# Kernel tuning notes

Measured on AMD Instinct MI355X. Metric: run time of the kernel, lower is better.

The kernel has to match this reference:

```python
import jax, jax.numpy as jnp
import numpy as np

B, DIM, H, W = 8, 128, 64, 64
HEADS = 8
NUMS = DIM // HEADS   # 16
OUT = 256

def setup_inputs() -> dict:
    key = jax.random.key(0)
    k1, k2, k3, k4, k5 = jax.random.split(key, 5)
    x = jax.random.normal(k1, (B, DIM, H, W), dtype=jnp.float32)
    # per-group 1x1 conv (num_heads -> 1): weight [nums, heads], bias [nums]
    W1 = jax.random.normal(k2, (NUMS, HEADS), dtype=jnp.float32) * (1.0 / np.sqrt(HEADS))
    b1 = jax.random.normal(k3, (NUMS,), dtype=jnp.float32) * 0.01
    # final 1x1 conv (nums*dim -> out_dim): weight [out, nums*dim], bias [out]
    W2 = jax.random.normal(k4, (OUT, NUMS * DIM), dtype=jnp.float32) * (1.0 / np.sqrt(NUMS * DIM))
    b2 = jax.random.normal(k5, (OUT,), dtype=jnp.float32) * 0.01
    return {"x": x, "W1": W1, "b1": b1, "W2": W2, "b2": b2}

def reference(x, W1, b1, W2, b2):
    B_, C, H_, W_ = x.shape
    # split channels into nums groups of num_heads: [B, nums, heads, H, W]
    xg = x.reshape(B_, NUMS, HEADS, H_, W_)
    # per-group 1x1 conv to 1 channel + ReLU -> attention maps [B, nums, H, W]
    fm = jax.nn.relu(jnp.einsum('bghxy,gh->bgxy', xg, W1) + b1[None, :, None, None])
    # broadcast-multiply each map against full x, concat -> [B, nums*dim, H, W]
    feat = (fm[:, :, None, :, :] * x[:, None, :, :, :]).reshape(B_, NUMS * C, H_, W_)
    # final 1x1 conv -> [B, out_dim, H, W]
    out = jnp.einsum('bcxy,oc->boxy', feat, W2) + b2[None, :, None, None]
    return out
```

## Files before the change

kernel.cpp:

```cpp
#include <hip/hip_runtime.h>

typedef float f32x4 __attribute__((ext_vector_type(4)));
typedef int   i32x4 __attribute__((ext_vector_type(4)));
typedef unsigned int u32;

#define HW_N  4096
#define C_N   128
#define G_N   16
#define K_N   2048
#define O_N   256
#define BN    128

__device__ __forceinline__ u32 pack4(float a, float b, float c, float d, float inv) {
  int q0 = (int)rintf(a * inv), q1 = (int)rintf(b * inv);
  int q2 = (int)rintf(c * inv), q3 = (int)rintf(d * inv);
  return (u32)(q0 & 255) | ((u32)(q1 & 255) << 8) |
         ((u32)(q2 & 255) << 16) | ((u32)(q3 & 255) << 24);
}

__global__ void w2q_k(const float* __restrict__ W2, char* __restrict__ w2q,
                      float* __restrict__ sw) {
  int o = (blockIdx.x * 256 + threadIdx.x) >> 6;
  int l = threadIdx.x & 63;
  const f32x4* rp = reinterpret_cast<const f32x4*>(W2 + (size_t)o * K_N + l * 32);
  float v[32]; float am = 0.f;
#pragma unroll
  for (int q = 0; q < 8; ++q) {
    f32x4 t = rp[q];
#pragma unroll
    for (int j = 0; j < 4; ++j) { v[q * 4 + j] = t[j]; am = fmaxf(am, fabsf(t[j])); }
  }
#pragma unroll
  for (int s = 1; s < 64; s <<= 1) am = fmaxf(am, __shfl_xor(am, s, 64));
  am = fmaxf(am, 1e-30f);
  float inv = 127.0f / am;
  if (l == 0) sw[o] = am / 127.0f;
#pragma unroll
  for (int c = 0; c < 2; ++c) {
    int k0 = l * 32 + c * 16;
    u32 pk[4];
#pragma unroll
    for (int q = 0; q < 4; ++q)
      pk[q] = pack4(v[c * 16 + q * 4 + 0], v[c * 16 + q * 4 + 1],
                    v[c * 16 + q * 4 + 2], v[c * 16 + q * 4 + 3], inv);
    int frag = (o >> 4) * 32 + (k0 >> 7) * 2 + ((k0 >> 6) & 1);
    int lif  = (o & 15) + ((k0 >> 4) & 3) * 16;
    *reinterpret_cast<i32x4*>(w2q + (size_t)frag * 1024 + lif * 16) =
        *reinterpret_cast<i32x4*>(pk);
  }
}

__launch_bounds__(256, 2)
__global__ void ccattn_main_k(const float* __restrict__ x,
                              const float* __restrict__ W1,
                              const float* __restrict__ b1,
                              const char* __restrict__ w2q,
                              const float* __restrict__ sw,
                              const float* __restrict__ b2,
                              float* __restrict__ out) {
  __shared__ char  qxT[BN * 128];
  __shared__ float fmT[G_N][BN];
  __shared__ float sxT[BN];
  __shared__ float lmax[2][BN];

  const int tid = threadIdx.x;
  const int bid = blockIdx.x;
  const int mt  = bid >> 8;
  const int pt  = bid & 255;
  const int b   = pt >> 5;
  const int px0 = (pt & 31) * BN;

  const float* xb = x + (size_t)b * C_N * HW_N + px0;

  const int px    = tid & 127;
  const int chalf = tid >> 7;
  float v[8][8];
  {
    float am = 0.f;
#pragma unroll
    for (int gg = 0; gg < 8; ++gg) {
      const int g  = chalf * 8 + gg;
      const int c0 = g * 8;
      float s = b1[g];
#pragma unroll
      for (int j = 0; j < 8; ++j) {
        float t = xb[(size_t)(c0 + j) * HW_N + px];
        v[gg][j] = t;
        s += t * W1[g * 8 + j];
        am = fmaxf(am, fabsf(t));
      }
      fmT[g][px] = fmaxf(s, 0.0f);
    }
    lmax[chalf][px] = am;
  }
  __syncthreads();

  {
    float amax = fmaxf(fmaxf(lmax[0][px], lmax[1][px]), 1e-30f);
    float inv  = 127.0f / amax;
    if (!chalf) sxT[px] = amax / 127.0f;
#pragma unroll
    for (int gr = 0; gr < 4; ++gr) {
      u32 pk[4];
#pragma unroll
      for (int q = 0; q < 4; ++q) {
        const int gg = gr * 2 + (q >> 1);
        const int j0 = (q & 1) * 4;
        pk[q] = pack4(v[gg][j0], v[gg][j0 + 1], v[gg][j0 + 2], v[gg][j0 + 3], inv);
      }
      int gidx = chalf * 4 + gr;
      int byte = px * 128 + ((gidx ^ (px & 7)) << 4);
      *reinterpret_cast<i32x4*>(qxT + byte) = *reinterpret_cast<i32x4*>(pk);
    }
  }
  __syncthreads();

  const int w  = tid >> 6;
  const int l  = tid & 63;
  const int wm = w & 1;
  const int wn = w >> 1;
  const int lc = l & 15;
  const int lk = l >> 4;

  i32x4 bfr[2][4];
#pragma unroll
  for (int ks2 = 0; ks2 < 2; ++ks2)
#pragma unroll
    for (int nf = 0; nf < 4; ++nf) {
      int p    = wn * 64 + nf * 16 + lc;
      int gidx = ks2 * 4 + lk;
      int byte = p * 128 + ((gidx ^ (p & 7)) << 4);
      bfr[ks2][nf] = *reinterpret_cast<const i32x4*>(qxT + byte);
    }

  f32x4 acc[4][4];
  const f32x4 Z = {0.f, 0.f, 0.f, 0.f};
#pragma unroll
  for (int mf = 0; mf < 4; ++mf)
#pragma unroll
    for (int nf = 0; nf < 4; ++nf) acc[mf][nf] = Z;

  const char* abm = w2q + (size_t)(mt * 8 + wm * 4) * 32768 + l * 16;

  i32x4 A0[8], A1[8];
  float snC[4], snN[4];

#define LDG(dst, g)                                                          \
  {                                                                          \
    _Pragma("unroll")                                                        \
    for (int mf = 0; mf < 4; ++mf) {                                         \
      dst[mf * 2]     = *reinterpret_cast<const i32x4*>(abm + (size_t)mf * 32768 + (g) * 2048);        \
      dst[mf * 2 + 1] = *reinterpret_cast<const i32x4*>(abm + (size_t)mf * 32768 + (g) * 2048 + 1024); \
    }                                                                        \
  }
#define LDSN(dst, g)                                                         \
  {                                                                          \
    _Pragma("unroll")                                                        \
    for (int nf = 0; nf < 4; ++nf) dst[nf] = fmT[g][wn * 64 + nf * 16 + lc]; \
  }
#define COMP(buf, sn)                                                        \
  {                                                                          \
    __builtin_amdgcn_s_setprio(1);                                           \
    _Pragma("unroll")                                                        \
    for (int nf = 0; nf < 4; ++nf) {                                         \
      i32x4 P[4];                                                            \
      _Pragma("unroll")                                                      \
      for (int mf = 0; mf < 4; ++mf)                                         \
        P[mf] = __builtin_amdgcn_mfma_i32_16x16x64_i8(                       \
            buf[mf * 2], bfr[0][nf], (i32x4){0, 0, 0, 0}, 0, 0, 0);          \
      _Pragma("unroll")                                                      \
      for (int mf = 0; mf < 4; ++mf)                                         \
        P[mf] = __builtin_amdgcn_mfma_i32_16x16x64_i8(                       \
            buf[mf * 2 + 1], bfr[1][nf], P[mf], 0, 0, 0);                    \
      _Pragma("unroll")                                                      \
      for (int mf = 0; mf < 4; ++mf) {                                       \
        _Pragma("unroll")                                                    \
        for (int i = 0; i < 4; ++i)                                          \
          acc[mf][nf][i] += sn[nf] * (float)P[mf][i];                        \
      }                                                                      \
    }                                                                        \
    __builtin_amdgcn_s_setprio(0);                                           \
  }

  LDG(A0, 0)
  LDSN(snC, 0)

#pragma unroll 1
  for (int g = 0; g < 16; g += 2) {
    LDG(A1, g + 1)
    LDSN(snN, g + 1)
    COMP(A0, snC)
    const int g2 = (g + 2 < 16) ? g + 2 : 15;
    LDG(A0, g2)
    LDSN(snC, g2)
    COMP(A1, snN)
  }
#undef LDG
#undef LDSN
#undef COMP

  float sxv[4];
#pragma unroll
  for (int nf = 0; nf < 4; ++nf) sxv[nf] = sxT[wn * 64 + nf * 16 + lc];
  float* outb = out + (size_t)b * O_N * HW_N + px0;
#pragma unroll
  for (int mf = 0; mf < 4; ++mf) {
    int o0 = mt * 128 + wm * 64 + mf * 16 + lk * 4;
#pragma unroll
    for (int i = 0; i < 4; ++i) {
      float so   = sw[o0 + i];
      float bias = b2[o0 + i];
#pragma unroll
      for (int nf = 0; nf < 4; ++nf) {
        int p = wn * 64 + nf * 16 + lc;
        outb[(size_t)(o0 + i) * HW_N + p] = acc[mf][nf][i] * so * sxv[nf] + bias;
      }
    }
  }
}

extern "C" void kernel_launch(void* const* d_in, const int* in_sizes, int n_in,
                              void* d_out, int out_size, void* d_ws, size_t ws_size,
                              hipStream_t stream) {
  const float* x  = (const float*)d_in[0];
  const float* W1 = (const float*)d_in[1];
  const float* b1 = (const float*)d_in[2];
  const float* W2 = (const float*)d_in[3];
  const float* b2 = (const float*)d_in[4];
  float* out = (float*)d_out;
  char*  w2q = (char*)d_ws;
  float* sw  = (float*)((char*)d_ws + 524288);

  w2q_k<<<64, 256, 0, stream>>>(W2, w2q, sw);
  ccattn_main_k<<<512, 256, 0, stream>>>(x, W1, b1, w2q, sw, b2, out);
}
```

Measured before the change: 40.20 us.

## Stage int8 W2 tiles into a double-buffered LDS via global_load_lds

Each wave now stops loading its own int8 W2 fragments from global memory into registers. The block cooperatively copies each group's 16KB W2 slice into a two-slot LDS buffer with direct global-to-LDS loads, and waves read their fragments from LDS. The quantized W2 layout is reordered so each group's slice is contiguous, and the quantization kernel launch is reshaped to one wave per output row. This removes duplicate global reads across waves that share the same M rows. In exchange it adds about 32KB of LDS per block and a block-wide barrier per group iteration, and it relies on the barrier also enforcing completion of the async LDS loads.

```diff
diff --git a/kernel.cpp b/kernel.cpp
--- a/kernel.cpp
+++ b/kernel.cpp
@@ -11,6 +11,9 @@
 #define O_N   256
 #define BN    128
 
+typedef const __attribute__((address_space(1))) u32 gbl_u32;
+typedef __attribute__((address_space(3))) u32 lds_u32;
+
 __device__ __forceinline__ u32 pack4(float a, float b, float c, float d, float inv) {
   int q0 = (int)rintf(a * inv), q1 = (int)rintf(b * inv);
   int q2 = (int)rintf(c * inv), q3 = (int)rintf(d * inv);
@@ -20,8 +23,8 @@
 
 __global__ void w2q_k(const float* __restrict__ W2, char* __restrict__ w2q,
                       float* __restrict__ sw) {
-  int o = (blockIdx.x * 256 + threadIdx.x) >> 6;
-  int l = threadIdx.x & 63;
+  int o = blockIdx.x;
+  int l = threadIdx.x;
   const f32x4* rp = reinterpret_cast<const f32x4*>(W2 + (size_t)o * K_N + l * 32);
   float v[32]; float am = 0.f;
 #pragma unroll
@@ -43,10 +46,11 @@
     for (int q = 0; q < 4; ++q)
       pk[q] = pack4(v[c * 16 + q * 4 + 0], v[c * 16 + q * 4 + 1],
                     v[c * 16 + q * 4 + 2], v[c * 16 + q * 4 + 3], inv);
-    int frag = (o >> 4) * 32 + (k0 >> 7) * 2 + ((k0 >> 6) & 1);
-    int lif  = (o & 15) + ((k0 >> 4) & 3) * 16;
-    *reinterpret_cast<i32x4*>(w2q + (size_t)frag * 1024 + lif * 16) =
-        *reinterpret_cast<i32x4*>(pk);
+    int g   = k0 >> 7;
+    int ks2 = (k0 >> 6) & 1;
+    int lif = (o & 15) + ((k0 >> 4) & 3) * 16;
+    *reinterpret_cast<i32x4*>(w2q + (size_t)g * 32768 + (o >> 4) * 2048 +
+                              ks2 * 1024 + lif * 16) = *reinterpret_cast<i32x4*>(pk);
   }
 }
 
@@ -58,6 +62,7 @@
                               const float* __restrict__ sw,
                               const float* __restrict__ b2,
                               float* __restrict__ out) {
+  __shared__ __align__(16) char Albs[2][16384];
   __shared__ char  qxT[BN * 128];
   __shared__ float fmT[G_N][BN];
   __shared__ float sxT[BN];
@@ -70,6 +75,20 @@
   const int b   = pt >> 5;
   const int px0 = (pt & 31) * BN;
 
+  const int w = tid >> 6;
+  const int l = tid & 63;
+
+  auto stage = [&](int g, int slot) {
+    const char* src = w2q + (size_t)g * 32768 + mt * 16384 + w * 4096 + l * 16;
+    char* dst = &Albs[slot][w * 4096];
+#pragma unroll
+    for (int r = 0; r < 4; ++r)
+      __builtin_amdgcn_global_load_lds((gbl_u32*)(src + r * 1024),
+                                       (lds_u32*)(dst + r * 1024), 16, 0, 0);
+  };
+  stage(0, 0);
+  stage(1, 1);
+
   const float* xb = x + (size_t)b * C_N * HW_N + px0;
 
   const int px    = tid & 127;
@@ -115,8 +134,6 @@
   }
   __syncthreads();
 
-  const int w  = tid >> 6;
-  const int l  = tid & 63;
   const int wm = w & 1;
   const int wn = w >> 1;
   const int lc = l & 15;
@@ -134,70 +151,48 @@
     }
 
   f32x4 acc[4][4];
-  const f32x4 Z = {0.f, 0.f, 0.f, 0.f};
 #pragma unroll
   for (int mf = 0; mf < 4; ++mf)
 #pragma unroll
-    for (int nf = 0; nf < 4; ++nf) acc[mf][nf] = Z;
-
-  const char* abm = w2q + (size_t)(mt * 8 + wm * 4) * 32768 + l * 16;
-
-  i32x4 A0[8], A1[8];
-  float snC[4], snN[4];
-
-#define LDG(dst, g)                                                          \
-  {                                                                          \
-    _Pragma("unroll")                                                        \
-    for (int mf = 0; mf < 4; ++mf) {                                         \
-      dst[mf * 2]     = *reinterpret_cast<const i32x4*>(abm + (size_t)mf * 32768 + (g) * 2048);        \
-      dst[mf * 2 + 1] = *reinterpret_cast<const i32x4*>(abm + (size_t)mf * 32768 + (g) * 2048 + 1024); \
-    }                                                                        \
-  }
-#define LDSN(dst, g)                                                         \
-  {                                                                          \
-    _Pragma("unroll")                                                        \
-    for (int nf = 0; nf < 4; ++nf) dst[nf] = fmT[g][wn * 64 + nf * 16 + lc]; \
-  }
-#define COMP(buf, sn)                                                        \
-  {                                                                          \
-    __builtin_amdgcn_s_setprio(1);                                           \
-    _Pragma("unroll")                                                        \
-    for (int nf = 0; nf < 4; ++nf) {                                         \
-      i32x4 P[4];                                                            \
-      _Pragma("unroll")                                                      \
-      for (int mf = 0; mf < 4; ++mf)                                         \
-        P[mf] = __builtin_amdgcn_mfma_i32_16x16x64_i8(                       \
-            buf[mf * 2], bfr[0][nf], (i32x4){0, 0, 0, 0}, 0, 0, 0);          \
-      _Pragma("unroll")                                                      \
-      for (int mf = 0; mf < 4; ++mf)                                         \
-        P[mf] = __builtin_amdgcn_mfma_i32_16x16x64_i8(                       \
-            buf[mf * 2 + 1], bfr[1][nf], P[mf], 0, 0, 0);                    \
-      _Pragma("unroll")                                                      \
-      for (int mf = 0; mf < 4; ++mf) {                                       \
-        _Pragma("unroll")                                                    \
-        for (int i = 0; i < 4; ++i)                                          \
-          acc[mf][nf][i] += sn[nf] * (float)P[mf][i];                        \
-      }                                                                      \
-    }                                                                        \
-    __builtin_amdgcn_s_setprio(0);                                           \
-  }
-
-  LDG(A0, 0)
-  LDSN(snC, 0)
+    for (int nf = 0; nf < 4; ++nf) acc[mf][nf] = (f32x4){0.f, 0.f, 0.f, 0.f};
 
 #pragma unroll 1
-  for (int g = 0; g < 16; g += 2) {
-    LDG(A1, g + 1)
-    LDSN(snN, g + 1)
-    COMP(A0, snC)
-    const int g2 = (g + 2 < 16) ? g + 2 : 15;
-    LDG(A0, g2)
-    LDSN(snC, g2)
-    COMP(A1, snN)
-  }
-#undef LDG
-#undef LDSN
-#undef COMP
+  for (int g = 0; g < 16; ++g) {
+    const char* ab = &Albs[g & 1][(size_t)wm * 8192];
+    i32x4 afr[8];
+#pragma unroll
+    for (int mf = 0; mf < 4; ++mf) {
+      afr[mf * 2]     = *reinterpret_cast<const i32x4*>(ab + mf * 2048 + l * 16);
+      afr[mf * 2 + 1] = *reinterpret_cast<const i32x4*>(ab + mf * 2048 + 1024 + l * 16);
+    }
+    float sn[4];
+#pragma unroll
+    for (int nf = 0; nf < 4; ++nf) sn[nf] = fmT[g][wn * 64 + nf * 16 + lc];
+
+    __builtin_amdgcn_s_setprio(1);
+#pragma unroll
+    for (int nf = 0; nf < 4; ++nf) {
+      i32x4 P[4];
+#pragma unroll
+      for (int mf = 0; mf < 4; ++mf)
+        P[mf] = __builtin_amdgcn_mfma_i32_16x16x64_i8(
+            afr[mf * 2], bfr[0][nf], (i32x4){0, 0, 0, 0}, 0, 0, 0);
+#pragma unroll
+      for (int mf = 0; mf < 4; ++mf)
+        P[mf] = __builtin_amdgcn_mfma_i32_16x16x64_i8(
+            afr[mf * 2 + 1], bfr[1][nf], P[mf], 0, 0, 0);
+#pragma unroll
+      for (int mf = 0; mf < 4; ++mf) {
+#pragma unroll
+        for (int i = 0; i < 4; ++i)
+          acc[mf][nf][i] += sn[nf] * (float)P[mf][i];
+      }
+    }
+    __builtin_amdgcn_s_setprio(0);
+
+    __syncthreads();
+    if (g + 2 < 16) stage(g + 2, g & 1);
+  }
 
   float sxv[4];
 #pragma unroll
@@ -231,6 +226,6 @@
   char*  w2q = (char*)d_ws;
   float* sw  = (float*)((char*)d_ws + 524288);
 
-  w2q_k<<<64, 256, 0, stream>>>(W2, w2q, sw);
+  w2q_k<<<256, 64, 0, stream>>>(W2, w2q, sw);
   ccattn_main_k<<<512, 256, 0, stream>>>(x, W1, b1, w2q, sw, b2, out);
 }
```

Measured after the change: 36.73 us. -8.6%, faster.
